# Optimization experiments

Measured on AMD Instinct MI355X. Metric: run time of the kernel, lower is better.

## Reference

```python
import jax, jax.numpy as jnp
import numpy as np

WEIGHT_BITS = 8
INPUT_BITS = 8


def fake_quant(t, bits):
    """Per-tensor symmetric absmax fake quantization with straight-through estimator."""
    qmax = 2.0 ** (bits - 1) - 1.0  # e.g. 127 for 8 bits
    scale = jnp.maximum(jnp.max(jnp.abs(t)), 1e-8) / qmax
    q = jnp.round(t / scale) * scale
    return t + jax.lax.stop_gradient(q - t)


def setup_inputs() -> dict:
    key = jax.random.key(0)
    k0, k1, k2, k3 = jax.random.split(key, 4)
    d, f, n = 4096, 11008, 4096
    s_in = 1.0 / np.sqrt(d)
    s_ff = 1.0 / np.sqrt(f)
    return {
        "x": jax.random.normal(k0, (n, d), jnp.float32),
        "w1": jax.random.normal(k1, (f, d), jnp.float32) * s_in,  # fc1: embed -> ffn
        "w3": jax.random.normal(k2, (f, d), jnp.float32) * s_in,  # fc3: gate proj
        "w2": jax.random.normal(k3, (d, f), jnp.float32) * s_ff,  # fc2: ffn -> embed
    }


def reference(x, w1, w3, w2):
    # quantized fc3 -> silu gate
    xq = fake_quant(x, INPUT_BITS)
    gate = jax.nn.silu(jnp.einsum('nd,fd->nf', xq, fake_quant(w3, WEIGHT_BITS)))
    # quantized fc1, multiplied by gate (GLU)
    h = jnp.einsum('nd,fd->nf', xq, fake_quant(w1, WEIGHT_BITS)) * gate
    # subln=False -> no ffn_layernorm; dropout=0 (eval)
    hq = fake_quant(h, INPUT_BITS)
    out = jnp.einsum('nf,df->nd', hq, fake_quant(w2, WEIGHT_BITS))
    return out
```

## Files before the change

kernel.cpp:

```cpp
#include <hip/hip_runtime.h>
#include <hip/hip_bf16.h>

typedef __attribute__((ext_vector_type(4))) int int4v;

#define MFMA_I8(a, b, c) __builtin_amdgcn_mfma_i32_16x16x64_i8((a), (b), (c), 0, 0, 0)
#define GLDS16(g, l)                                                                        \
  __builtin_amdgcn_global_load_lds((const __attribute__((address_space(1))) void*)(g),      \
                                   (__attribute__((address_space(3))) void*)(l), 16, 0, 0)
#define SBAR() __builtin_amdgcn_s_barrier()
#define SCHED0() __builtin_amdgcn_sched_barrier(0)

static constexpr int NTOK = 4096;
static constexpr int DDIM = 4096;
static constexpr int FDIM = 11008;


__device__ __forceinline__ float wave_max64(float m) {
#pragma unroll
  for (int o = 32; o > 0; o >>= 1) m = fmaxf(m, __shfl_xor(m, o));
  return m;
}

__global__ void zero_slots(unsigned* s) {
  if (threadIdx.x < 16) s[threadIdx.x] = 0u;
}

__device__ __forceinline__ void absmax_body(const float* __restrict__ p, int n4,
                                            unsigned* __restrict__ slot) {
  float m = 0.f;
  const int stride = gridDim.x * blockDim.x;
  for (int i = blockIdx.x * blockDim.x + threadIdx.x; i < n4; i += stride) {
    float4 v = reinterpret_cast<const float4*>(p)[i];
    m = fmaxf(fmaxf(fabsf(v.x), fabsf(v.y)), fmaxf(fmaxf(fabsf(v.z), fabsf(v.w)), m));
  }
  m = wave_max64(m);
  __shared__ float wm[4];
  const int lane = threadIdx.x & 63, w = threadIdx.x >> 6;
  if (lane == 0) wm[w] = m;
  __syncthreads();
  if (threadIdx.x == 0) {
    m = fmaxf(fmaxf(wm[0], wm[1]), fmaxf(wm[2], wm[3]));
    atomicMax(slot, __float_as_uint(m));
  }
}

__global__ void absmax4(const float* x, const float* w1, const float* w3, const float* w2,
                        unsigned* slots, int n4x, int n4w) {
  const int seg = blockIdx.y;
  const float* p = (seg == 0) ? x : (seg == 1) ? w1 : (seg == 2) ? w3 : w2;
  absmax_body(p, seg == 0 ? n4x : n4w, slots + seg);
}

__device__ __forceinline__ void quant_body(const float* __restrict__ in,
                                           unsigned* __restrict__ out, int n4,
                                           const unsigned* __restrict__ slot) {
  const float s = fmaxf(__uint_as_float(*slot), 1e-8f) / 127.0f;
  const int stride = gridDim.x * blockDim.x;
  for (int i = blockIdx.x * blockDim.x + threadIdx.x; i < n4; i += stride) {
    float4 v = reinterpret_cast<const float4*>(in)[i];
    const int q0 = (int)rintf(v.x / s), q1 = (int)rintf(v.y / s);
    const int q2 = (int)rintf(v.z / s), q3 = (int)rintf(v.w / s);
    out[i] = (unsigned)(q0 & 255) | ((unsigned)(q1 & 255) << 8) |
             ((unsigned)(q2 & 255) << 16) | ((unsigned)(q3 & 255) << 24);
  }
}

__global__ void quant4(const float* x, const float* w1, const float* w3, const float* w2,
                       unsigned* qx, unsigned* qw1, unsigned* qw3, unsigned* qw2,
                       const unsigned* slots, int n4x, int n4w) {
  const int seg = blockIdx.y;
  const float* p = (seg == 0) ? x : (seg == 1) ? w1 : (seg == 2) ? w3 : w2;
  unsigned* o = (seg == 0) ? qx : (seg == 1) ? qw1 : (seg == 2) ? qw3 : qw2;
  quant_body(p, o, seg == 0 ? n4x : n4w, slots + seg);
}

__global__ void quant_kernel(const float* __restrict__ in, unsigned* __restrict__ out,
                             int n4, const unsigned* __restrict__ slot) {
  quant_body(in, out, n4, slot);
}

__global__ __launch_bounds__(512, 2) void gemm_glu(
    const signed char* __restrict__ Aq, const signed char* __restrict__ B3q,
    const signed char* __restrict__ B1q, float* __restrict__ H,
    const unsigned* __restrict__ slots, unsigned* __restrict__ hslot) {
  constexpr int K = DDIM;
  __shared__ char lds[163840];

  const int t = threadIdx.x;
  const int l = t & 63;
  const int w = t >> 6;
  const int wm = w >> 2;
  const int wn = w & 3;

  const int gx = gridDim.x, gy = gridDim.y;
  const int nwg = gx * gy;
  const int i0 = blockIdx.y * gx + blockIdx.x;
  const int cid = (i0 & 7) * (nwg >> 3) + (i0 >> 3);
  const int rowA0 = (cid % gy) << 7;
  const int colB0 = (cid / gy) << 8;

  const int rl = t >> 3;
  const int gl = (t & 7) ^ (rl & 7);
  const signed char* aP = Aq + (size_t)(rowA0 + rl) * K + gl * 16;
  const signed char* b3P = B3q + (size_t)(colB0 + rl) * K + gl * 16;
  const signed char* b1P = B1q + (size_t)(colB0 + rl) * K + gl * 16;
  const size_t r64 = (size_t)64 * K;
  const int stW = w * 1024;

#define STAGE10(KO, BASE)                                            \
  do {                                                               \
    GLDS16(aP + (KO), &lds[(BASE) + stW]);                           \
    GLDS16(aP + r64 + (KO), &lds[(BASE) + 8192 + stW]);              \
    GLDS16(b3P + (KO), &lds[(BASE) + 16384 + stW]);                  \
    GLDS16(b3P + r64 + (KO), &lds[(BASE) + 24576 + stW]);            \
    GLDS16(b3P + 2 * r64 + (KO), &lds[(BASE) + 32768 + stW]);        \
    GLDS16(b3P + 3 * r64 + (KO), &lds[(BASE) + 40960 + stW]);        \
    GLDS16(b1P + (KO), &lds[(BASE) + 49152 + stW]);                  \
    GLDS16(b1P + r64 + (KO), &lds[(BASE) + 57344 + stW]);            \
    GLDS16(b1P + 2 * r64 + (KO), &lds[(BASE) + 65536 + stW]);        \
    GLDS16(b1P + 3 * r64 + (KO), &lds[(BASE) + 73728 + stW]);        \
  } while (0)

#define LDSF(BASE, ROW, G)                                                    \
  (*reinterpret_cast<const int4v*>(                                           \
      &lds[(BASE) + (ROW)*128 + (((G) ^ ((ROW)&7)) << 4)]))

  int4v acc3[4][4], acc1[4][4];
#pragma unroll
  for (int m = 0; m < 4; ++m)
#pragma unroll
    for (int n = 0; n < 4; ++n) {
      acc3[m][n] = (int4v){0, 0, 0, 0};
      acc1[m][n] = (int4v){0, 0, 0, 0};
    }

  const int NT = K >> 7;
  const int arow = wm * 64 + (l & 15);
  const int brow = wn * 64 + (l & 15);
  const int cr = l >> 4;

  STAGE10(0, 0);

  for (int kt = 0; kt < NT; ++kt) {
    const int rb = (kt & 1) * 81920;
    SCHED0();
    asm volatile("s_waitcnt vmcnt(0)" ::: "memory");
    SBAR();
    SCHED0();

    if (kt + 1 < NT) STAGE10((size_t)(kt + 1) * 128, rb ^ 81920);

#pragma unroll
    for (int kk = 0; kk < 2; ++kk) {
      int4v a[4], b3f[4], b1f[4];
#pragma unroll
      for (int m = 0; m < 4; ++m) a[m] = LDSF(rb, arow + m * 16, kk * 4 + cr);
#pragma unroll
      for (int n = 0; n < 4; ++n) b3f[n] = LDSF(rb + 16384, brow + n * 16, kk * 4 + cr);
#pragma unroll
      for (int n = 0; n < 4; ++n) b1f[n] = LDSF(rb + 49152, brow + n * 16, kk * 4 + cr);
      __builtin_amdgcn_s_setprio(1);
#pragma unroll
      for (int m = 0; m < 4; ++m)
#pragma unroll
        for (int n = 0; n < 4; ++n) acc3[m][n] = MFMA_I8(a[m], b3f[n], acc3[m][n]);
#pragma unroll
      for (int m = 0; m < 4; ++m)
#pragma unroll
        for (int n = 0; n < 4; ++n) acc1[m][n] = MFMA_I8(a[m], b1f[n], acc1[m][n]);
      __builtin_amdgcn_s_setprio(0);
    }
  }

  const float sx = fmaxf(__uint_as_float(slots[0]), 1e-8f) / 127.0f;
  const float sw1 = fmaxf(__uint_as_float(slots[1]), 1e-8f) / 127.0f;
  const float sw3 = fmaxf(__uint_as_float(slots[2]), 1e-8f) / 127.0f;
  const float s3 = sx * sw3, s1 = sx * sw1;
  const int crow0 = rowA0 + wm * 64 + ((l >> 4) << 2);
  const int ccol0 = colB0 + wn * 64 + (l & 15);
  float hmax = 0.f;
#pragma unroll
  for (int m = 0; m < 4; ++m)
#pragma unroll
    for (int n = 0; n < 4; ++n)
#pragma unroll
      for (int j = 0; j < 4; ++j) {
        const int row = crow0 + m * 16 + j;
        const int col = ccol0 + n * 16;
        const float g = (float)acc3[m][n][j] * s3;
        const float gate = g / (1.f + expf(-g));
        const float h = (float)acc1[m][n][j] * s1 * gate;
        H[(size_t)row * FDIM + col] = h;
        hmax = fmaxf(hmax, fabsf(h));
      }
  hmax = wave_max64(hmax);
  if (l == 0) atomicMax(hslot, __float_as_uint(hmax));
#undef STAGE10
#undef LDSF
}

__global__ __launch_bounds__(512, 2) void gemm_down(
    const signed char* __restrict__ Aq, const signed char* __restrict__ Bq,
    float* __restrict__ C, const unsigned* __restrict__ slots, int sA, int sB,
    int K, int ldc) {
  __shared__ char lds[131072];

  const int t = threadIdx.x;
  const int l = t & 63;
  const int w = t >> 6;
  const int wm = w >> 2;
  const int wn = w & 3;

  const int gx = gridDim.x, gy = gridDim.y;
  const int nwg = gx * gy;
  const int i0 = blockIdx.y * gx + blockIdx.x;
  const int cid = (i0 & 7) * (nwg >> 3) + (i0 >> 3);
  const int rowA0 = (cid % gy) << 8;
  const int colB0 = (cid / gy) << 8;

  const int rl = t >> 3;
  const int gl = (t & 7) ^ (rl & 7);
  const signed char* aP = Aq + (size_t)(rowA0 + rl) * K + gl * 16;
  const signed char* bP = Bq + (size_t)(colB0 + rl) * K + gl * 16;
  const size_t r64 = (size_t)64 * K;
  const int stW = w * 1024;

#define STAGE8(KO, BASE)                                             \
  do {                                                               \
    GLDS16(aP + (KO), &lds[(BASE) + stW]);                           \
    GLDS16(aP + r64 + (KO), &lds[(BASE) + 8192 + stW]);              \
    GLDS16(aP + 2 * r64 + (KO), &lds[(BASE) + 16384 + stW]);         \
    GLDS16(aP + 3 * r64 + (KO), &lds[(BASE) + 24576 + stW]);         \
    GLDS16(bP + (KO), &lds[(BASE) + 32768 + stW]);                   \
    GLDS16(bP + r64 + (KO), &lds[(BASE) + 40960 + stW]);             \
    GLDS16(bP + 2 * r64 + (KO), &lds[(BASE) + 49152 + stW]);         \
    GLDS16(bP + 3 * r64 + (KO), &lds[(BASE) + 57344 + stW]);         \
  } while (0)

#define LDSF(BASE, ROW, G)                                                    \
  (*reinterpret_cast<const int4v*>(                                           \
      &lds[(BASE) + (ROW)*128 + (((G) ^ ((ROW)&7)) << 4)]))

  int4v acc[8][4];
#pragma unroll
  for (int m = 0; m < 8; ++m)
#pragma unroll
    for (int n = 0; n < 4; ++n) acc[m][n] = (int4v){0, 0, 0, 0};

  const int NT = K >> 7;
  const int arow = wm * 128 + (l & 15);
  const int brow = wn * 64 + (l & 15);
  const int cr = l >> 4;

  STAGE8(0, 0);

  for (int kt = 0; kt < NT; ++kt) {
    const int rb = (kt & 1) * 65536;
    SCHED0();
    asm volatile("s_waitcnt vmcnt(0)" ::: "memory");
    SBAR();
    SCHED0();

    if (kt + 1 < NT) STAGE8((size_t)(kt + 1) * 128, rb ^ 65536);

#pragma unroll
    for (int kk = 0; kk < 2; ++kk) {
      int4v a[8], b[4];
#pragma unroll
      for (int m = 0; m < 8; ++m) a[m] = LDSF(rb, arow + m * 16, kk * 4 + cr);
#pragma unroll
      for (int n = 0; n < 4; ++n) b[n] = LDSF(rb + 32768, brow + n * 16, kk * 4 + cr);
      __builtin_amdgcn_s_setprio(1);
#pragma unroll
      for (int m = 0; m < 8; ++m)
#pragma unroll
        for (int n = 0; n < 4; ++n) acc[m][n] = MFMA_I8(a[m], b[n], acc[m][n]);
      __builtin_amdgcn_s_setprio(0);
    }
  }

  const float sa = fmaxf(__uint_as_float(slots[sA]), 1e-8f) / 127.0f;
  const float sb2 = fmaxf(__uint_as_float(slots[sB]), 1e-8f) / 127.0f;
  const float s = sa * sb2;
  const int crow0 = rowA0 + wm * 128 + ((l >> 4) << 2);
  const int ccol0 = colB0 + wn * 64 + (l & 15);
#pragma unroll
  for (int m = 0; m < 8; ++m)
#pragma unroll
    for (int n = 0; n < 4; ++n)
#pragma unroll
      for (int j = 0; j < 4; ++j) {
        const int row = crow0 + m * 16 + j;
        const int col = ccol0 + n * 16;
        C[(size_t)row * ldc + col] = (float)acc[m][n][j] * s;
      }
#undef STAGE8
#undef LDSF
}


extern "C" void kernel_launch(void* const* d_in, const int* in_sizes, int n_in,
                              void* d_out, int out_size, void* d_ws, size_t ws_size,
                              hipStream_t stream) {
  const float* x = (const float*)d_in[0];
  const float* w1 = (const float*)d_in[1];
  const float* w3 = (const float*)d_in[2];
  const float* w2 = (const float*)d_in[3];
  float* out = (float*)d_out;
  char* ws = (char*)d_ws;

  unsigned* slots = (unsigned*)ws;
  size_t off = 256;
  signed char* qx = (signed char*)(ws + off);
  off += (size_t)NTOK * DDIM;
  signed char* qw3 = (signed char*)(ws + off);
  off += (size_t)FDIM * DDIM;
  signed char* qw1 = (signed char*)(ws + off);
  off += (size_t)FDIM * DDIM;
  signed char* qw2 = (signed char*)(ws + off);
  off += (size_t)FDIM * DDIM;
  float* H = (float*)(ws + off);
  off += (size_t)NTOK * FDIM * 4;
  signed char* qh = (signed char*)(ws + off);
  off += (size_t)NTOK * FDIM;

  const int n4x = NTOK * DDIM / 4;
  const int n4w = FDIM * DDIM / 4;
  const int n4h = NTOK * FDIM / 4;

  zero_slots<<<1, 64, 0, stream>>>(slots);
  absmax4<<<dim3(512, 4), 256, 0, stream>>>(x, w1, w3, w2, slots, n4x, n4w);
  quant4<<<dim3(512, 4), 256, 0, stream>>>(x, w1, w3, w2, (unsigned*)qx, (unsigned*)qw1,
                                           (unsigned*)qw3, (unsigned*)qw2, slots, n4x, n4w);

  const dim3 gGlu(FDIM / 256, NTOK / 128);
  gemm_glu<<<gGlu, 512, 0, stream>>>(qx, qw3, qw1, H, slots, slots + 4);
  quant_kernel<<<2048, 256, 0, stream>>>(H, (unsigned*)qh, n4h, slots + 4);
  const dim3 gDn(DDIM / 256, NTOK / 256);
  gemm_down<<<gDn, 512, 0, stream>>>(qh, qw2, out, slots, 4, 3, FDIM, DDIM);
}
```

Measured before the change: 906.7 us.

## Re-tile GLU GEMM waves to 128x32 with per-wave B staging and split waits

Changes the gemm_glu wave layout from a 2x4 grid of 64x64 tiles to eight waves each owning all 128 rows and a 32-column slice. Each wave now loads its own B3/B1 slice into LDS, so only the shared A tile has to wait on the workgroup barrier. The per-wave B loads are waited on later with partial vmcnt counts, which lets the A fragment reads overlap with B loads still in flight. MFMAs for the gate and up projections are interleaved over two k-halves. The risks are more LDS fragment reads of A per wave and subtle correctness issues in the vmcnt accounting.

```diff
diff --git a/kernel.cpp b/kernel.cpp
--- a/kernel.cpp
+++ b/kernel.cpp
@@ -89,8 +89,6 @@
   const int t = threadIdx.x;
   const int l = t & 63;
   const int w = t >> 6;
-  const int wm = w >> 2;
-  const int wn = w & 3;
 
   const int gx = gridDim.x, gy = gridDim.y;
   const int nwg = gx * gy;
@@ -99,90 +97,128 @@
   const int rowA0 = (cid % gy) << 7;
   const int colB0 = (cid / gy) << 8;
 
-  const int rl = t >> 3;
-  const int gl = (t & 7) ^ (rl & 7);
-  const signed char* aP = Aq + (size_t)(rowA0 + rl) * K + gl * 16;
-  const signed char* b3P = B3q + (size_t)(colB0 + rl) * K + gl * 16;
-  const signed char* b1P = B1q + (size_t)(colB0 + rl) * K + gl * 16;
+  const int rlA = t >> 3;
+  const int glA = (t & 7) ^ (rlA & 7);
+  const signed char* aP = Aq + (size_t)(rowA0 + rlA) * K + glA * 16;
   const size_t r64 = (size_t)64 * K;
   const int stW = w * 1024;
 
-#define STAGE10(KO, BASE)                                            \
-  do {                                                               \
-    GLDS16(aP + (KO), &lds[(BASE) + stW]);                           \
-    GLDS16(aP + r64 + (KO), &lds[(BASE) + 8192 + stW]);              \
-    GLDS16(b3P + (KO), &lds[(BASE) + 16384 + stW]);                  \
-    GLDS16(b3P + r64 + (KO), &lds[(BASE) + 24576 + stW]);            \
-    GLDS16(b3P + 2 * r64 + (KO), &lds[(BASE) + 32768 + stW]);        \
-    GLDS16(b3P + 3 * r64 + (KO), &lds[(BASE) + 40960 + stW]);        \
-    GLDS16(b1P + (KO), &lds[(BASE) + 49152 + stW]);                  \
-    GLDS16(b1P + r64 + (KO), &lds[(BASE) + 57344 + stW]);            \
-    GLDS16(b1P + 2 * r64 + (KO), &lds[(BASE) + 65536 + stW]);        \
-    GLDS16(b1P + 3 * r64 + (KO), &lds[(BASE) + 73728 + stW]);        \
+  const int rlB = l >> 3;
+  const int glB = (l & 7) ^ rlB;
+  const signed char* b3P = B3q + (size_t)(colB0 + w * 32 + rlB) * K + glB * 16;
+  const signed char* b1P = B1q + (size_t)(colB0 + w * 32 + rlB) * K + glB * 16;
+  const size_t r8 = (size_t)8 * K;
+  const int bBase3 = 16384 + w * 4096;
+  const int bBase1 = 49152 + w * 4096;
+
+#define STAGE_A(KO, BUF)                            \
+  do {                                              \
+    GLDS16(aP + (KO), &lds[(BUF) + stW]);           \
+    GLDS16(aP + r64 + (KO), &lds[(BUF) + 8192 + stW]); \
   } while (0)
 
-#define LDSF(BASE, ROW, G)                                                    \
+#define STAGE_B(KO, BUF)                                           \
+  do {                                                             \
+    GLDS16(b3P + (KO), &lds[(BUF) + bBase3]);                      \
+    GLDS16(b3P + r8 + (KO), &lds[(BUF) + bBase3 + 1024]);          \
+    GLDS16(b3P + 2 * r8 + (KO), &lds[(BUF) + bBase3 + 2048]);      \
+    GLDS16(b3P + 3 * r8 + (KO), &lds[(BUF) + bBase3 + 3072]);      \
+    GLDS16(b1P + (KO), &lds[(BUF) + bBase1]);                      \
+    GLDS16(b1P + r8 + (KO), &lds[(BUF) + bBase1 + 1024]);          \
+    GLDS16(b1P + 2 * r8 + (KO), &lds[(BUF) + bBase1 + 2048]);      \
+    GLDS16(b1P + 3 * r8 + (KO), &lds[(BUF) + bBase1 + 3072]);      \
+  } while (0)
+
+#define LDSF(BASE, R, G)                                                      \
   (*reinterpret_cast<const int4v*>(                                           \
-      &lds[(BASE) + (ROW)*128 + (((G) ^ ((ROW)&7)) << 4)]))
-
-  int4v acc3[4][4], acc1[4][4];
-#pragma unroll
-  for (int m = 0; m < 4; ++m)
-#pragma unroll
-    for (int n = 0; n < 4; ++n) {
+      &lds[(BASE) + (R)*128 + (((G) ^ ((R)&7)) << 4)]))
+
+  int4v acc3[8][2], acc1[8][2];
+#pragma unroll
+  for (int m = 0; m < 8; ++m)
+#pragma unroll
+    for (int n = 0; n < 2; ++n) {
       acc3[m][n] = (int4v){0, 0, 0, 0};
       acc1[m][n] = (int4v){0, 0, 0, 0};
     }
 
   const int NT = K >> 7;
-  const int arow = wm * 64 + (l & 15);
-  const int brow = wn * 64 + (l & 15);
+  const int lr = l & 15;
   const int cr = l >> 4;
 
-  STAGE10(0, 0);
+  STAGE_A(0, 0);
+  STAGE_B(0, 0);
 
   for (int kt = 0; kt < NT; ++kt) {
     const int rb = (kt & 1) * 81920;
-    SCHED0();
-    asm volatile("s_waitcnt vmcnt(0)" ::: "memory");
+    const bool haveNext = (kt + 1 < NT);
+
+    SCHED0();
+    asm volatile("s_waitcnt vmcnt(8)" ::: "memory");
     SBAR();
     SCHED0();
 
-    if (kt + 1 < NT) STAGE10((size_t)(kt + 1) * 128, rb ^ 81920);
-
-#pragma unroll
-    for (int kk = 0; kk < 2; ++kk) {
-      int4v a[4], b3f[4], b1f[4];
-#pragma unroll
-      for (int m = 0; m < 4; ++m) a[m] = LDSF(rb, arow + m * 16, kk * 4 + cr);
-#pragma unroll
-      for (int n = 0; n < 4; ++n) b3f[n] = LDSF(rb + 16384, brow + n * 16, kk * 4 + cr);
-#pragma unroll
-      for (int n = 0; n < 4; ++n) b1f[n] = LDSF(rb + 49152, brow + n * 16, kk * 4 + cr);
-      __builtin_amdgcn_s_setprio(1);
-#pragma unroll
-      for (int m = 0; m < 4; ++m)
-#pragma unroll
-        for (int n = 0; n < 4; ++n) acc3[m][n] = MFMA_I8(a[m], b3f[n], acc3[m][n]);
-#pragma unroll
-      for (int m = 0; m < 4; ++m)
-#pragma unroll
-        for (int n = 0; n < 4; ++n) acc1[m][n] = MFMA_I8(a[m], b1f[n], acc1[m][n]);
-      __builtin_amdgcn_s_setprio(0);
-    }
+    if (haveNext) {
+      const size_t kO = (size_t)(kt + 1) * 128;
+      STAGE_A(kO, rb ^ 81920);
+      STAGE_B(kO, rb ^ 81920);
+    }
+
+    int4v a[8];
+#pragma unroll
+    for (int m = 0; m < 8; ++m) a[m] = LDSF(rb, m * 16 + lr, cr);
+
+    if (haveNext) {
+      asm volatile("s_waitcnt vmcnt(10)" ::: "memory");
+    } else {
+      asm volatile("s_waitcnt vmcnt(0)" ::: "memory");
+    }
+    SCHED0();
+
+    int4v b3f[2][2], b1f[2][2];
+#pragma unroll
+    for (int n = 0; n < 2; ++n) {
+      const int R = n * 16 + lr;
+      b3f[0][n] = LDSF(rb + bBase3, R, cr);
+      b3f[1][n] = LDSF(rb + bBase3, R, 4 + cr);
+      b1f[0][n] = LDSF(rb + bBase1, R, cr);
+      b1f[1][n] = LDSF(rb + bBase1, R, 4 + cr);
+    }
+
+    __builtin_amdgcn_s_setprio(1);
+#pragma unroll
+    for (int m = 0; m < 8; ++m)
+#pragma unroll
+      for (int n = 0; n < 2; ++n) {
+        acc3[m][n] = MFMA_I8(a[m], b3f[0][n], acc3[m][n]);
+        acc1[m][n] = MFMA_I8(a[m], b1f[0][n], acc1[m][n]);
+      }
+    __builtin_amdgcn_s_setprio(0);
+
+#pragma unroll
+    for (int m = 0; m < 8; ++m) a[m] = LDSF(rb, m * 16 + lr, 4 + cr);
+    __builtin_amdgcn_s_setprio(1);
+#pragma unroll
+    for (int m = 0; m < 8; ++m)
+#pragma unroll
+      for (int n = 0; n < 2; ++n) {
+        acc3[m][n] = MFMA_I8(a[m], b3f[1][n], acc3[m][n]);
+        acc1[m][n] = MFMA_I8(a[m], b1f[1][n], acc1[m][n]);
+      }
+    __builtin_amdgcn_s_setprio(0);
   }
 
   const float sx = fmaxf(__uint_as_float(slots[0]), 1e-8f) / 127.0f;
   const float sw1 = fmaxf(__uint_as_float(slots[1]), 1e-8f) / 127.0f;
   const float sw3 = fmaxf(__uint_as_float(slots[2]), 1e-8f) / 127.0f;
   const float s3 = sx * sw3, s1 = sx * sw1;
-  const int crow0 = rowA0 + wm * 64 + ((l >> 4) << 2);
-  const int ccol0 = colB0 + wn * 64 + (l & 15);
+  const int crow0 = rowA0 + ((l >> 4) << 2);
+  const int ccol0 = colB0 + w * 32 + lr;
   float hmax = 0.f;
 #pragma unroll
-  for (int m = 0; m < 4; ++m)
-#pragma unroll
-    for (int n = 0; n < 4; ++n)
+  for (int m = 0; m < 8; ++m)
+#pragma unroll
+    for (int n = 0; n < 2; ++n)
 #pragma unroll
       for (int j = 0; j < 4; ++j) {
         const int row = crow0 + m * 16 + j;
@@ -195,7 +231,8 @@
       }
   hmax = wave_max64(hmax);
   if (l == 0) atomicMax(hslot, __float_as_uint(hmax));
-#undef STAGE10
+#undef STAGE_A
+#undef STAGE_B
 #undef LDSF
 }
 
```

New measurement: 893.0 us. Within noise of the previous version (-1.5%).
